# Optimization experiments

Measured on AMD Instinct MI355X. Metric: run time of the kernel, lower is better.

Reference implementation:

```python
import jax, jax.numpy as jnp
import numpy as np

B = 16384
I = 1024  # inputs_size
H = 1024  # hidden_size


def _linear_params(key, fan_in, fan_out):
    # torch nn.Linear default init: U(-1/sqrt(fan_in), 1/sqrt(fan_in))
    kw, kb = jax.random.split(key)
    bound = 1.0 / np.sqrt(fan_in)
    W = jax.random.uniform(kw, (fan_out, fan_in), jnp.float32, -bound, bound)
    b = jax.random.uniform(kb, (fan_out,), jnp.float32, -bound, bound)
    return W, b


def setup_inputs() -> dict:
    key = jax.random.key(0)
    ks = jax.random.split(key, 8)
    inp = {
        "input": jax.random.normal(ks[0], (B, I), jnp.float32),
        "hidden": jax.random.normal(ks[1], (B, H), jnp.float32),
    }
    names = ["r_i", "r_h", "z_i", "z_h", "n_i", "n_h"]
    fan_ins = [I, H, I, H, I, H]
    for name, fi, k in zip(names, fan_ins, ks[2:]):
        W, b = _linear_params(k, fi, H)
        inp[f"W_{name}"] = W
        inp[f"b_{name}"] = b
    return inp


def reference(input, hidden,
              W_r_i, b_r_i, W_r_h, b_r_h,
              W_z_i, b_z_i, W_z_h, b_z_h,
              W_n_i, b_n_i, W_n_h, b_n_h):
    # Faithful to the original (including its bug: z uses r_layer_h(hidden)).
    r_h = hidden @ W_r_h.T + b_r_h  # reused by both r and z gates
    r = jax.nn.sigmoid(input @ W_r_i.T + b_r_i + r_h)
    z = jax.nn.sigmoid(input @ W_z_i.T + b_z_i + r_h)
    n = jnp.tanh(input @ W_n_i.T + b_n_i + r * (hidden @ W_n_h.T + b_n_h))
    next_hidden = (1.0 - z) * n + z * hidden
    return (next_hidden, next_hidden)
```

## Files before the change

kernel.cpp:

```cpp
#include <hip/hip_runtime.h>


#define BM 128
#define BN 64
#define BK 32
#define TILE_BYTES 36864

typedef __attribute__((ext_vector_type(8))) short          bf16x8;
typedef __attribute__((ext_vector_type(8))) unsigned short u16x8;
typedef __attribute__((ext_vector_type(4))) float          f32x4;

__device__ __forceinline__ unsigned short f2bf(float f) {
    union { float f; unsigned u; } v; v.f = f;
    unsigned r = v.u + 0x7FFFu + ((v.u >> 16) & 1u);
    return (unsigned short)(r >> 16);
}

__global__ __launch_bounds__(256) void convert_bf16(
    const float* __restrict__ in0, const float* __restrict__ in1,
    const float* __restrict__ w0, const float* __restrict__ w1,
    const float* __restrict__ w2, const float* __restrict__ w3,
    const float* __restrict__ w4, unsigned short* __restrict__ ws)
{
    const long long e = ((long long)blockIdx.x * 256 + threadIdx.x) * 8;
    const float* src;
    if (e < 16777216LL) {
        src = in0 + e;
    } else if (e < 33554432LL) {
        src = in1 + (e - 16777216LL);
    } else {
        const long long t = e - 33554432LL;
        const int g = (int)(t >> 20);
        const long long within = t & 1048575LL;
        const float* w = (g == 0) ? w0 : (g == 1) ? w1 : (g == 2) ? w2 : (g == 3) ? w3 : w4;
        src = w + within;
    }
    const float4 a = *reinterpret_cast<const float4*>(src);
    const float4 b = *reinterpret_cast<const float4*>(src + 4);
    u16x8 o;
    o[0] = f2bf(a.x); o[1] = f2bf(a.y); o[2] = f2bf(a.z); o[3] = f2bf(a.w);
    o[4] = f2bf(b.x); o[5] = f2bf(b.y); o[6] = f2bf(b.z); o[7] = f2bf(b.w);
    *reinterpret_cast<u16x8*>(ws + e) = o;
}

__device__ __forceinline__ void async16(const void* g, void* l) {
    __builtin_amdgcn_global_load_lds(
        (const __attribute__((address_space(1))) unsigned int*)g,
        (__attribute__((address_space(3))) unsigned int*)l, 16, 0, 0);
}

#define CFENCE() asm volatile("" ::: "memory")

__global__ __launch_bounds__(256, 2) void gru_fused(
    const unsigned short* __restrict__ bf,
    const float* __restrict__ hidden,
    const float* __restrict__ b_ri, const float* __restrict__ b_rh,
    const float* __restrict__ b_zi, const float* __restrict__ b_ni,
    const float* __restrict__ b_nh,
    float* __restrict__ out)
{
    const int H = 1024, K = 1024;
    const int BH = 16384 * 1024;

    __shared__ __align__(16) unsigned char sBuf[2][TILE_BYTES];

    const int tid  = threadIdx.x;
    const int wave = tid >> 6;
    const int lane = tid & 63;
    const int quad = lane >> 4;
    const int l16  = lane & 15;
    const int sq   = quad ^ ((l16 >> 1) & 3);
    const int wm   = wave >> 1;
    const int wn   = wave & 1;

    const int f   = blockIdx.y * gridDim.x + blockIdx.x;
    const int lin = (f & 7) * 256 + (f >> 3);
    const int bx  = lin >> 7;
    const int by  = lin & 127;

    const int row0 = by * BM;
    const int col0 = bx * BN;

    const unsigned short* inB  = bf;
    const unsigned short* hidB = bf + 16777216;
    const unsigned short* wB   = bf + 33554432;

    const unsigned short* srcbase[9];
    int ldsoff[9];
    #pragma unroll
    for (int j = 0; j < 9; ++j) {
        const int s = (j * 4 + wave) * 64 + lane;
        ldsoff[j] = s * 16;
        if (s < 512) {
            const int r = s >> 2;
            const int c = (s & 3) ^ ((r >> 1) & 3);
            srcbase[j] = inB + (long long)(row0 + r) * K + c * 8;
        } else if (s < 1024) {
            const int r = (s - 512) >> 2;
            const int c = (s & 3) ^ ((r >> 1) & 3);
            srcbase[j] = hidB + (long long)(row0 + r) * K + c * 8;
        } else {
            const int t = s - 1024;
            const int g = t >> 8;
            const int tt = t & 255;
            const int n = tt >> 2;
            const int c = (tt & 3) ^ ((n >> 1) & 3);
            srcbase[j] = wB + (long long)g * 1048576 + (long long)(col0 + n) * K + c * 8;
        }
    }

    f32x4 acc[5][4][2];
    #pragma unroll
    for (int g = 0; g < 5; ++g)
        #pragma unroll
        for (int mi = 0; mi < 4; ++mi)
            #pragma unroll
            for (int ni = 0; ni < 2; ++ni)
                acc[g][mi][ni] = (f32x4){0.f, 0.f, 0.f, 0.f};

    unsigned char* b0 = &sBuf[0][0];
    unsigned char* b1 = &sBuf[1][0];

    auto stage = [&](int k0, unsigned char* dst) {
        #pragma unroll
        for (int j = 0; j < 9; ++j)
            async16(srcbase[j] + k0, dst + ldsoff[j]);
    };

    auto compute = [&](const unsigned char* sb) {
        bf16x8 aIn[4], aHid[4];
        #pragma unroll
        for (int mi = 0; mi < 4; ++mi) {
            const int r = wm * 64 + mi * 16 + l16;
            aIn [mi] = *reinterpret_cast<const bf16x8*>(sb + r * 64 + sq * 16);
            aHid[mi] = *reinterpret_cast<const bf16x8*>(sb + 8192 + r * 64 + sq * 16);
        }
        __builtin_amdgcn_s_setprio(1);
        #pragma unroll
        for (int g = 0; g < 5; ++g) {
            #pragma unroll
            for (int ni = 0; ni < 2; ++ni) {
                const int n = wn * 32 + ni * 16 + l16;
                const bf16x8 b = *reinterpret_cast<const bf16x8*>(
                    sb + 16384 + g * 4096 + n * 64 + sq * 16);
                #pragma unroll
                for (int mi = 0; mi < 4; ++mi) {
                    const bf16x8 a = (g == 1 || g == 4) ? aHid[mi] : aIn[mi];
                    acc[g][mi][ni] = __builtin_amdgcn_mfma_f32_16x16x32_bf16(a, b, acc[g][mi][ni], 0, 0, 0);
                }
            }
        }
        __builtin_amdgcn_s_setprio(0);
    };

    stage(0, b0);
    #pragma unroll 1
    for (int i = 0; i < 15; ++i) {
        const int k2 = i * 2 * BK;
        stage(k2 + BK, b1);
        asm volatile("s_waitcnt vmcnt(9)" ::: "memory");
        __builtin_amdgcn_s_barrier(); CFENCE();
        compute(b0); CFENCE();
        __builtin_amdgcn_s_barrier(); CFENCE();

        stage(k2 + 2 * BK, b0);
        asm volatile("s_waitcnt vmcnt(9)" ::: "memory");
        __builtin_amdgcn_s_barrier(); CFENCE();
        compute(b1); CFENCE();
        __builtin_amdgcn_s_barrier(); CFENCE();
    }
    stage(31 * BK, b1);
    asm volatile("s_waitcnt vmcnt(9)" ::: "memory");
    __builtin_amdgcn_s_barrier(); CFENCE();
    compute(b0); CFENCE();
    __builtin_amdgcn_s_barrier(); CFENCE();
    asm volatile("s_waitcnt vmcnt(0)" ::: "memory");
    __builtin_amdgcn_s_barrier(); CFENCE();
    compute(b1);

    #pragma unroll
    for (int ni = 0; ni < 2; ++ni) {
        const int gcol = col0 + wn * 32 + ni * 16 + l16;
        const float bri = b_ri[gcol], brh = b_rh[gcol], bzi = b_zi[gcol];
        const float bni = b_ni[gcol], bnh = b_nh[gcol];
        #pragma unroll
        for (int mi = 0; mi < 4; ++mi) {
            #pragma unroll
            for (int r4 = 0; r4 < 4; ++r4) {
                const int grow = row0 + wm * 64 + mi * 16 + quad * 4 + r4;
                const float g_ri = acc[0][mi][ni][r4];
                const float g_rh = acc[1][mi][ni][r4];
                const float g_zi = acc[2][mi][ni][r4];
                const float g_ni = acc[3][mi][ni][r4];
                const float g_nh = acc[4][mi][ni][r4];
                const float rh = g_rh + brh;
                const float rr = 1.f / (1.f + __expf(-(g_ri + bri + rh)));
                const float zz = 1.f / (1.f + __expf(-(g_zi + bzi + rh)));
                const float nn = tanhf(g_ni + bni + rr * (g_nh + bnh));
                const float h  = hidden[(long long)grow * H + gcol];
                const float o  = (1.f - zz) * nn + zz * h;
                out[(long long)grow * H + gcol]      = o;
                out[BH + (long long)grow * H + gcol] = o;
            }
        }
    }
}

extern "C" void kernel_launch(void* const* d_in, const int* in_sizes, int n_in,
                              void* d_out, int out_size, void* d_ws, size_t ws_size,
                              hipStream_t stream) {
    const float* input  = (const float*)d_in[0];
    const float* hidden = (const float*)d_in[1];
    const float* W_ri = (const float*)d_in[2];
    const float* b_ri = (const float*)d_in[3];
    const float* W_rh = (const float*)d_in[4];
    const float* b_rh = (const float*)d_in[5];
    const float* W_zi = (const float*)d_in[6];
    const float* b_zi = (const float*)d_in[7];
    const float* W_ni = (const float*)d_in[10];
    const float* b_ni = (const float*)d_in[11];
    const float* W_nh = (const float*)d_in[12];
    const float* b_nh = (const float*)d_in[13];
    float* out = (float*)d_out;
    unsigned short* ws = (unsigned short*)d_ws;

    convert_bf16<<<18944, 256, 0, stream>>>(input, hidden, W_ri, W_rh, W_zi, W_ni, W_nh, ws);

    dim3 grid(1024 / BN, 16384 / BM);
    gru_fused<<<grid, 256, 0, stream>>>(ws, hidden, b_ri, b_rh, b_zi, b_ni, b_nh, out);
}
```

Measured before the change: 504.5 us.

## Double block tile to 256 rows with 8 waves and phased per-gate LDS pipeline

Doubles the M tile to 256 rows and uses 512-thread blocks, so each weight tile is shared by twice as many rows. The compute step is split into three gate phases, each with its own LDS loads and barriers, and the next stage's loads are issued only after compute on that buffer finishes. The block swizzle is dropped, global offsets become 32-bit, and each convert thread now handles two units. The goal is more reuse and more overlap, at the cost of many extra barriers, higher LDS use per block, and possibly lower occupancy and L2 locality.

```diff
diff --git a/kernel.cpp b/kernel.cpp
--- a/kernel.cpp
+++ b/kernel.cpp
@@ -1,10 +1,10 @@
 #include <hip/hip_runtime.h>
 
 
-#define BM 128
+#define BM 256
 #define BN 64
 #define BK 32
-#define TILE_BYTES 36864
+#define TILE_BYTES 53248
 
 typedef __attribute__((ext_vector_type(8))) short          bf16x8;
 typedef __attribute__((ext_vector_type(8))) unsigned short u16x8;
@@ -16,13 +16,14 @@
     return (unsigned short)(r >> 16);
 }
 
-__global__ __launch_bounds__(256) void convert_bf16(
+__device__ __forceinline__ void cvt_unit(
+    long long u,
     const float* __restrict__ in0, const float* __restrict__ in1,
     const float* __restrict__ w0, const float* __restrict__ w1,
     const float* __restrict__ w2, const float* __restrict__ w3,
     const float* __restrict__ w4, unsigned short* __restrict__ ws)
 {
-    const long long e = ((long long)blockIdx.x * 256 + threadIdx.x) * 8;
+    const long long e = u * 8;
     const float* src;
     if (e < 16777216LL) {
         src = in0 + e;
@@ -43,6 +44,17 @@
     *reinterpret_cast<u16x8*>(ws + e) = o;
 }
 
+__global__ __launch_bounds__(256) void convert_bf16(
+    const float* __restrict__ in0, const float* __restrict__ in1,
+    const float* __restrict__ w0, const float* __restrict__ w1,
+    const float* __restrict__ w2, const float* __restrict__ w3,
+    const float* __restrict__ w4, unsigned short* __restrict__ ws)
+{
+    const long long u = (long long)blockIdx.x * 256 + threadIdx.x;
+    cvt_unit(u,             in0, in1, w0, w1, w2, w3, w4, ws);
+    cvt_unit(u + 2424832LL, in0, in1, w0, w1, w2, w3, w4, ws);
+}
+
 __device__ __forceinline__ void async16(const void* g, void* l) {
     __builtin_amdgcn_global_load_lds(
         (const __attribute__((address_space(1))) unsigned int*)g,
@@ -50,8 +62,9 @@
 }
 
 #define CFENCE() asm volatile("" ::: "memory")
-
-__global__ __launch_bounds__(256, 2) void gru_fused(
+#define MFMA16(a, b, c) __builtin_amdgcn_mfma_f32_16x16x32_bf16((a), (b), (c), 0, 0, 0)
+
+__global__ __launch_bounds__(512, 2) void gru_fused(
     const unsigned short* __restrict__ bf,
     const float* __restrict__ hidden,
     const float* __restrict__ b_ri, const float* __restrict__ b_rh,
@@ -73,41 +86,42 @@
     const int wm   = wave >> 1;
     const int wn   = wave & 1;
 
-    const int f   = blockIdx.y * gridDim.x + blockIdx.x;
-    const int lin = (f & 7) * 256 + (f >> 3);
-    const int bx  = lin >> 7;
-    const int by  = lin & 127;
-
-    const int row0 = by * BM;
-    const int col0 = bx * BN;
-
-    const unsigned short* inB  = bf;
-    const unsigned short* hidB = bf + 16777216;
-    const unsigned short* wB   = bf + 33554432;
-
-    const unsigned short* srcbase[9];
-    int ldsoff[9];
+    const int row0 = blockIdx.y * BM;
+    const int col0 = blockIdx.x * BN;
+
+    unsigned srcoff[7];
     #pragma unroll
-    for (int j = 0; j < 9; ++j) {
-        const int s = (j * 4 + wave) * 64 + lane;
-        ldsoff[j] = s * 16;
-        if (s < 512) {
-            const int r = s >> 2;
-            const int c = (s & 3) ^ ((r >> 1) & 3);
-            srcbase[j] = inB + (long long)(row0 + r) * K + c * 8;
-        } else if (s < 1024) {
-            const int r = (s - 512) >> 2;
-            const int c = (s & 3) ^ ((r >> 1) & 3);
-            srcbase[j] = hidB + (long long)(row0 + r) * K + c * 8;
-        } else {
-            const int t = s - 1024;
-            const int g = t >> 8;
-            const int tt = t & 255;
-            const int n = tt >> 2;
-            const int c = (tt & 3) ^ ((n >> 1) & 3);
-            srcbase[j] = wB + (long long)g * 1048576 + (long long)(col0 + n) * K + c * 8;
-        }
-    }
+    for (int j = 0; j < 7; ++j) {
+        if (j < 6 || tid < 256) {
+            const int s = j * 512 + tid;
+            if (s < 1024) {
+                const int r = s >> 2;
+                const int c = (s & 3) ^ ((r >> 1) & 3);
+                srcoff[j] = (unsigned)((row0 + r) * K + c * 8);
+            } else if (s < 2048) {
+                const int r = (s - 1024) >> 2;
+                const int c = ((s - 1024) & 3) ^ ((r >> 1) & 3);
+                srcoff[j] = (unsigned)(16777216 + (row0 + r) * K + c * 8);
+            } else {
+                const int t = s - 2048;
+                const int g = t >> 8;
+                const int tt = t & 255;
+                const int n = tt >> 2;
+                const int c = (tt & 3) ^ ((n >> 1) & 3);
+                srcoff[j] = (unsigned)(33554432u + g * 1048576u + (col0 + n) * K + c * 8);
+            }
+        }
+    }
+
+    auto stage = [&](int kofs, unsigned char* dst) {
+        #pragma unroll
+        for (int j = 0; j < 7; ++j)
+            if (j < 6 || tid < 256)
+                async16(bf + srcoff[j] + kofs, dst + j * 8192 + tid * 16);
+    };
+
+    #define WAIT_N() do { if (tid < 256) asm volatile("s_waitcnt vmcnt(7)" ::: "memory"); \
+                          else           asm volatile("s_waitcnt vmcnt(6)" ::: "memory"); } while (0)
 
     f32x4 acc[5][4][2];
     #pragma unroll
@@ -118,65 +132,101 @@
             for (int ni = 0; ni < 2; ++ni)
                 acc[g][mi][ni] = (f32x4){0.f, 0.f, 0.f, 0.f};
 
-    unsigned char* b0 = &sBuf[0][0];
-    unsigned char* b1 = &sBuf[1][0];
-
-    auto stage = [&](int k0, unsigned char* dst) {
-        #pragma unroll
-        for (int j = 0; j < 9; ++j)
-            async16(srcbase[j] + k0, dst + ldsoff[j]);
-    };
-
-    auto compute = [&](const unsigned char* sb) {
-        bf16x8 aIn[4], aHid[4];
+    unsigned char* B0 = &sBuf[0][0];
+    unsigned char* B1 = &sBuf[1][0];
+
+    auto tile = [&](const unsigned char* sb, int stage_k, unsigned char* stage_dst, int mode) {
+        bf16x8 aIn[4], aHid[4], bb0[2];
         #pragma unroll
         for (int mi = 0; mi < 4; ++mi) {
             const int r = wm * 64 + mi * 16 + l16;
             aIn [mi] = *reinterpret_cast<const bf16x8*>(sb + r * 64 + sq * 16);
-            aHid[mi] = *reinterpret_cast<const bf16x8*>(sb + 8192 + r * 64 + sq * 16);
-        }
+            aHid[mi] = *reinterpret_cast<const bf16x8*>(sb + 16384 + r * 64 + sq * 16);
+        }
+        #pragma unroll
+        for (int ni = 0; ni < 2; ++ni) {
+            const int n = wn * 32 + ni * 16 + l16;
+            bb0[ni] = *reinterpret_cast<const bf16x8*>(sb + 32768 + n * 64 + sq * 16);
+        }
+        CFENCE(); __builtin_amdgcn_s_barrier(); CFENCE();
+        asm volatile("s_waitcnt lgkmcnt(0)" ::: "memory");
         __builtin_amdgcn_s_setprio(1);
         #pragma unroll
-        for (int g = 0; g < 5; ++g) {
-            #pragma unroll
-            for (int ni = 0; ni < 2; ++ni) {
-                const int n = wn * 32 + ni * 16 + l16;
-                const bf16x8 b = *reinterpret_cast<const bf16x8*>(
-                    sb + 16384 + g * 4096 + n * 64 + sq * 16);
-                #pragma unroll
-                for (int mi = 0; mi < 4; ++mi) {
-                    const bf16x8 a = (g == 1 || g == 4) ? aHid[mi] : aIn[mi];
-                    acc[g][mi][ni] = __builtin_amdgcn_mfma_f32_16x16x32_bf16(a, b, acc[g][mi][ni], 0, 0, 0);
-                }
-            }
-        }
+        for (int ni = 0; ni < 2; ++ni)
+            #pragma unroll
+            for (int mi = 0; mi < 4; ++mi)
+                acc[0][mi][ni] = MFMA16(aIn[mi], bb0[ni], acc[0][mi][ni]);
         __builtin_amdgcn_s_setprio(0);
+        CFENCE(); __builtin_amdgcn_s_barrier(); CFENCE();
+
+        bf16x8 bb1[2], bb2[2];
+        #pragma unroll
+        for (int ni = 0; ni < 2; ++ni) {
+            const int n = wn * 32 + ni * 16 + l16;
+            bb1[ni] = *reinterpret_cast<const bf16x8*>(sb + 32768 + 4096 + n * 64 + sq * 16);
+            bb2[ni] = *reinterpret_cast<const bf16x8*>(sb + 32768 + 8192 + n * 64 + sq * 16);
+        }
+        CFENCE(); __builtin_amdgcn_s_barrier(); CFENCE();
+        asm volatile("s_waitcnt lgkmcnt(0)" ::: "memory");
+        __builtin_amdgcn_s_setprio(1);
+        #pragma unroll
+        for (int ni = 0; ni < 2; ++ni)
+            #pragma unroll
+            for (int mi = 0; mi < 4; ++mi)
+                acc[1][mi][ni] = MFMA16(aHid[mi], bb1[ni], acc[1][mi][ni]);
+        #pragma unroll
+        for (int ni = 0; ni < 2; ++ni)
+            #pragma unroll
+            for (int mi = 0; mi < 4; ++mi)
+                acc[2][mi][ni] = MFMA16(aIn[mi], bb2[ni], acc[2][mi][ni]);
+        __builtin_amdgcn_s_setprio(0);
+        CFENCE(); __builtin_amdgcn_s_barrier(); CFENCE();
+
+        bf16x8 bb3[2], bb4[2];
+        #pragma unroll
+        for (int ni = 0; ni < 2; ++ni) {
+            const int n = wn * 32 + ni * 16 + l16;
+            bb3[ni] = *reinterpret_cast<const bf16x8*>(sb + 32768 + 12288 + n * 64 + sq * 16);
+            bb4[ni] = *reinterpret_cast<const bf16x8*>(sb + 32768 + 16384 + n * 64 + sq * 16);
+        }
+        CFENCE(); __builtin_amdgcn_s_barrier(); CFENCE();
+        asm volatile("s_waitcnt lgkmcnt(0)" ::: "memory");
+        __builtin_amdgcn_s_setprio(1);
+        #pragma unroll
+        for (int ni = 0; ni < 2; ++ni)
+            #pragma unroll
+            for (int mi = 0; mi < 4; ++mi)
+                acc[3][mi][ni] = MFMA16(aIn[mi], bb3[ni], acc[3][mi][ni]);
+        #pragma unroll
+        for (int ni = 0; ni < 2; ++ni)
+            #pragma unroll
+            for (int mi = 0; mi < 4; ++mi)
+                acc[4][mi][ni] = MFMA16(aHid[mi], bb4[ni], acc[4][mi][ni]);
+        __builtin_amdgcn_s_setprio(0);
+        CFENCE(); __builtin_amdgcn_s_barrier(); CFENCE();
+
+        if (mode == 0) {
+            stage(stage_k, stage_dst);
+            WAIT_N();
+            CFENCE(); __builtin_amdgcn_s_barrier(); CFENCE();
+        } else if (mode == 1) {
+            asm volatile("s_waitcnt vmcnt(0)" ::: "memory");
+            CFENCE(); __builtin_amdgcn_s_barrier(); CFENCE();
+        }
     };
 
-    stage(0, b0);
+    stage(0,  B0);
+    stage(BK, B1);
+    WAIT_N();
+    CFENCE(); __builtin_amdgcn_s_barrier(); CFENCE();
+
     #pragma unroll 1
     for (int i = 0; i < 15; ++i) {
-        const int k2 = i * 2 * BK;
-        stage(k2 + BK, b1);
-        asm volatile("s_waitcnt vmcnt(9)" ::: "memory");
-        __builtin_amdgcn_s_barrier(); CFENCE();
-        compute(b0); CFENCE();
-        __builtin_amdgcn_s_barrier(); CFENCE();
-
-        stage(k2 + 2 * BK, b0);
-        asm volatile("s_waitcnt vmcnt(9)" ::: "memory");
-        __builtin_amdgcn_s_barrier(); CFENCE();
-        compute(b1); CFENCE();
-        __builtin_amdgcn_s_barrier(); CFENCE();
-    }
-    stage(31 * BK, b1);
-    asm volatile("s_waitcnt vmcnt(9)" ::: "memory");
-    __builtin_amdgcn_s_barrier(); CFENCE();
-    compute(b0); CFENCE();
-    __builtin_amdgcn_s_barrier(); CFENCE();
-    asm volatile("s_waitcnt vmcnt(0)" ::: "memory");
-    __builtin_amdgcn_s_barrier(); CFENCE();
-    compute(b1);
+        tile(B0, (2 * i + 2) * BK, B0, 0);
+        tile(B1, (2 * i + 3) * BK, B1, 0);
+    }
+    tile(B0, 0, nullptr, 1);
+    tile(B1, 0, nullptr, 2);
 
     #pragma unroll
     for (int ni = 0; ni < 2; ++ni) {
@@ -224,8 +274,8 @@
     float* out = (float*)d_out;
     unsigned short* ws = (unsigned short*)d_ws;
 
-    convert_bf16<<<18944, 256, 0, stream>>>(input, hidden, W_ri, W_rh, W_zi, W_ni, W_nh, ws);
+    convert_bf16<<<9472, 256, 0, stream>>>(input, hidden, W_ri, W_rh, W_zi, W_ni, W_nh, ws);
 
     dim3 grid(1024 / BN, 16384 / BM);
-    gru_fused<<<grid, 256, 0, stream>>>(ws, hidden, b_ri, b_rh, b_zi, b_ni, b_nh, out);
-}
+    gru_fused<<<grid, 512, 0, stream>>>(ws, hidden, b_ri, b_rh, b_zi, b_ni, b_nh, out);
+}
```

Result: slower. 517.1 us (+2.5%).
